# Performance work log

Hardware: AMD Instinct MI355X
Metric: run time of the kernel (lower is better)

The kernel has to match this reference:

```python
import jax, jax.numpy as jnp
import numpy as np

BATCH, NODE, IN_DIM, DIM, TOPK = 256, 256, 64, 64, 20
EPS = 1e-5
NEG_SLOPE = 0.2


def setup_inputs() -> dict:
    key = jax.random.key(0)
    ks = jax.random.split(key, 10)
    z, o = jnp.zeros, jnp.ones
    return {
        "data": jax.random.normal(ks[0], (BATCH, NODE, IN_DIM), jnp.float32),
        "emb_table": jax.random.normal(ks[1], (NODE, DIM), jnp.float32) * 0.1,
        "lin_w": jax.random.normal(ks[2], (IN_DIM, DIM), jnp.float32) * 0.05,
        "att_i": jax.random.normal(ks[3], (DIM,), jnp.float32) * 0.1,
        "att_j": jax.random.normal(ks[4], (DIM,), jnp.float32) * 0.1,
        "att_em_i": jax.random.normal(ks[5], (DIM,), jnp.float32) * 0.1,
        "att_em_j": jax.random.normal(ks[6], (DIM,), jnp.float32) * 0.1,
        "gnn_bias": z((DIM,), jnp.float32),
        "bn1_gamma": o((DIM,), jnp.float32), "bn1_beta": z((DIM,), jnp.float32),
        "bn2_gamma": o((DIM,), jnp.float32), "bn2_beta": z((DIM,), jnp.float32),
        "enc_w": jax.random.normal(ks[7], (NODE * DIM, DIM), jnp.float32) * 0.01,
        "enc_b": z((DIM,), jnp.float32),
        "arr_w": jax.random.normal(ks[8], (DIM, 7), jnp.float32) * 0.1,
        "arr_b": z((7,), jnp.float32),
        "out_w": jax.random.normal(ks[9], (DIM, 1), jnp.float32) * 0.1,
        "out_b": z((1,), jnp.float32),
    }


def _batchnorm(x, gamma, beta, axes):
    # BatchNorm1d in training mode: batch statistics
    mean = jnp.mean(x, axis=axes, keepdims=True)
    var = jnp.var(x, axis=axes, keepdims=True)
    return (x - mean) * jax.lax.rsqrt(var + EPS) * gamma + beta


def _gdn_forward(data, emb_table, lin_w, att_i, att_j, att_em_i, att_em_j, gnn_bias,
                 bn1_gamma, bn1_beta, bn2_gamma, bn2_beta,
                 enc_w, enc_b, arr_w, arr_b, out_w, out_b):
    B, N, F = data.shape
    BN = B * N
    x = data.reshape(BN, F)

    # learned graph: top-k cosine similarity of (detached) node embeddings
    w = jax.lax.stop_gradient(emb_table)
    nrm = jnp.linalg.norm(w, axis=-1)
    cos = (w @ w.T) / (nrm[:, None] * nrm[None, :])
    topk_idx = jax.lax.top_k(cos, TOPK)[1]                 # [N, TOPK]

    # gated_edge_index = (gated_j=sources, gated_i=targets), batched with +b*N offset
    src1 = topk_idx.reshape(-1)                            # sources (j)
    dst1 = jnp.repeat(jnp.arange(N), TOPK)                 # targets (i)
    offs = (jnp.arange(B) * N)[:, None]
    src = (src1[None, :] + offs).reshape(-1)               # [B*N*TOPK]
    dst = (dst1[None, :] + offs).reshape(-1)

    # PyG: remove_self_loops then add_self_loops -> mask duplicate self edges,
    # append exactly one self loop per node
    loop = jnp.arange(BN)
    src_all = jnp.concatenate([src, loop])
    dst_all = jnp.concatenate([dst, loop])
    valid = jnp.concatenate([src != dst, jnp.ones((BN,), bool)])

    # GraphLayer (GAT-style, heads=1, concat=False)
    xl = x @ lin_w                                         # [BN, DIM]
    emb_rep = jnp.tile(emb_table, (B, 1))                  # [BN, DIM] (embedding.repeat(B,1))
    x_i, x_j = xl[dst_all], xl[src_all]                    # per-edge gathers
    e_i, e_j = emb_rep[dst_all], emb_rep[src_all]
    logits = (x_i @ att_i) + (e_i @ att_em_i) + (x_j @ att_j) + (e_j @ att_em_j)
    logits = jnp.where(logits >= 0, logits, NEG_SLOPE * logits)  # leaky_relu(0.2)
    logits = jnp.where(valid, logits, -1e9)

    # segment softmax over incoming edges of each target node
    seg_max = jax.ops.segment_max(logits, dst_all, num_segments=BN)
    a = jnp.where(valid, jnp.exp(logits - seg_max[dst_all]), 0.0)
    denom = jax.ops.segment_sum(a, dst_all, num_segments=BN)
    alpha = a / denom[dst_all]

    # weighted scatter-add aggregation + bias, then GNNLayer BN + ReLU
    agg = jax.ops.segment_sum(x_j * alpha[:, None], dst_all, num_segments=BN) + gnn_bias
    gnn_out = jax.nn.relu(_batchnorm(agg, bn1_gamma, bn1_beta, axes=(0,)))

    x3 = gnn_out.reshape(B, N, -1)                         # [B, N, DIM]
    encoded = x3.reshape(B, -1) @ enc_w + enc_b            # [B, DIM]
    arrangement = encoded @ arr_w + arr_b                  # [B, 7]

    y = x3 * emb_table[None]                               # mul by node embeddings
    y = jnp.transpose(y, (0, 2, 1))                        # [B, DIM, N]
    y = jax.nn.relu(_batchnorm(y, bn2_gamma[None, :, None], bn2_beta[None, :, None], axes=(0, 2)))
    y = jnp.transpose(y, (0, 2, 1))                        # [B, N, DIM] (dropout is identity in eval)
    score = (y @ out_w + out_b).reshape(B, N)              # OutLayer (layer_num=1) + view(-1, N)
    return score, arrangement


def reference(data, emb_table, lin_w, att_i, att_j, att_em_i, att_em_j, gnn_bias,
              bn1_gamma, bn1_beta, bn2_gamma, bn2_beta,
              enc_w, enc_b, arr_w, arr_b, out_w, out_b):
    return _gdn_forward(data, emb_table, lin_w, att_i, att_j, att_em_i, att_em_j, gnn_bias,
                        bn1_gamma, bn1_beta, bn2_gamma, bn2_beta,
                        enc_w, enc_b, arr_w, arr_b, out_w, out_b)
```

## Files before the change

### kernel.cpp

```cpp
#include <hip/hip_runtime.h>
#include <hip/hip_bf16.h>

#define TK 20
#define BN 65536

typedef const float* fpc;
typedef __attribute__((ext_vector_type(8))) short short8;
typedef __attribute__((ext_vector_type(4))) float floatx4;

__device__ __forceinline__ short f2b(float f){
  unsigned u = __float_as_uint(f);
  return (short)((u + 0x7fffu + ((u >> 16) & 1u)) >> 16);
}
__device__ __forceinline__ float b2fu(unsigned short u){
  return __uint_as_float(((unsigned)u) << 16);
}

__global__ void __launch_bounds__(256) k_gx(fpc data, fpc emb, fpc lin_w, fpc att_i, fpc att_j,
        fpc att_em_i, fpc att_em_j,
        int* __restrict__ topk, float* __restrict__ emi, float* __restrict__ emj,
        __hip_bfloat16* __restrict__ xl, float* __restrict__ aip, float* __restrict__ ajp,
        float* __restrict__ bnsum){
  __shared__ float s_cos[256];
  __shared__ float s_wi[64];
  const int t = threadIdx.x, w = t >> 6, lane = t & 63;

  if (blockIdx.x < 256){
    if (blockIdx.x == 0){
      #pragma unroll
      for (int i = 0; i < 8; ++i) bnsum[t + i*256] = 0.f;
    }
    const int i = blockIdx.x;
    if (t < 64) s_wi[t] = emb[i*64 + t];
    __syncthreads();
    float dot = 0.f, nj = 0.f, ni = 0.f;
    for (int f = 0; f < 64; ++f){
      float wj = emb[t*64 + f], wi = s_wi[f];
      dot = fmaf(wi, wj, dot); nj = fmaf(wj, wj, nj); ni = fmaf(wi, wi, ni);
    }
    s_cos[t] = dot / (sqrtf(ni) * sqrtf(nj));
    __syncthreads();
    if (t < 64){
      float v0 = s_cos[t], v1 = s_cos[t+64], v2 = s_cos[t+128], v3 = s_cos[t+192];
      int taken = 0;
      for (int r = 0; r < TK; ++r){
        float bv = (taken & 1) ? -3.f : v0; int bi = t;
        float c;
        c = (taken & 2) ? -3.f : v1; if (c > bv){ bv = c; bi = t+64;  }
        c = (taken & 4) ? -3.f : v2; if (c > bv){ bv = c; bi = t+128; }
        c = (taken & 8) ? -3.f : v3; if (c > bv){ bv = c; bi = t+192; }
        for (int m = 1; m < 64; m <<= 1){
          float ov = __shfl_xor(bv, m, 64);
          int   oi = __shfl_xor(bi, m, 64);
          if (ov > bv || (ov == bv && oi < bi)){ bv = ov; bi = oi; }
        }
        if (t == 0) topk[i*TK + r] = bi;
        if ((bi & 63) == t) taken |= 1 << (bi >> 6);
      }
    } else if (t < 128){
      int d = t - 64;
      float wv = s_wi[d];
      float p1 = wv * att_em_i[d];
      float p2 = wv * att_em_j[d];
      for (int m = 1; m < 64; m <<= 1){
        p1 += __shfl_xor(p1, m, 64);
        p2 += __shfl_xor(p2, m, 64);
      }
      if (d == 0){ emi[i] = p1; emj[i] = p2; }
    }
    return;
  }

  const int m = lane & 15, quad = lane >> 4;
  short8 B[4][2];
  #pragma unroll
  for (int ct = 0; ct < 4; ++ct)
    #pragma unroll
    for (int kc = 0; kc < 2; ++kc)
      #pragma unroll
      for (int j = 0; j < 8; ++j)
        B[ct][kc][j] = f2b(lin_w[(kc*32 + quad*8 + j)*64 + ct*16 + m]);

  const int rw = (blockIdx.x - 256)*64 + w*16;
  short8 A0, A1;
  {
    const float4* ap0 = (const float4*)(data + (size_t)(rw + m)*64 + quad*8);
    float4 q0 = ap0[0], q1 = ap0[1];
    A0[0]=f2b(q0.x); A0[1]=f2b(q0.y); A0[2]=f2b(q0.z); A0[3]=f2b(q0.w);
    A0[4]=f2b(q1.x); A0[5]=f2b(q1.y); A0[6]=f2b(q1.z); A0[7]=f2b(q1.w);
    const float4* ap1 = (const float4*)(data + (size_t)(rw + m)*64 + 32 + quad*8);
    float4 q2 = ap1[0], q3 = ap1[1];
    A1[0]=f2b(q2.x); A1[1]=f2b(q2.y); A1[2]=f2b(q2.z); A1[3]=f2b(q2.w);
    A1[4]=f2b(q3.x); A1[5]=f2b(q3.y); A1[6]=f2b(q3.z); A1[7]=f2b(q3.w);
  }
  floatx4 acc[4];
  #pragma unroll
  for (int ct = 0; ct < 4; ++ct){
    floatx4 z = {0.f, 0.f, 0.f, 0.f};
    acc[ct] = __builtin_amdgcn_mfma_f32_16x16x32_bf16(A0, B[ct][0], z, 0, 0, 0);
    acc[ct] = __builtin_amdgcn_mfma_f32_16x16x32_bf16(A1, B[ct][1], acc[ct], 0, 0, 0);
  }
  float p1[4] = {0.f,0.f,0.f,0.f}, p2[4] = {0.f,0.f,0.f,0.f};
  #pragma unroll
  for (int ct = 0; ct < 4; ++ct){
    const float wi = att_i[ct*16 + m], wj = att_j[ct*16 + m];
    #pragma unroll
    for (int reg = 0; reg < 4; ++reg){
      float v = acc[ct][reg];
      const int row = rw + quad*4 + reg;
      xl[(size_t)row*64 + ct*16 + m] = __float2bfloat16(v);
      p1[reg] = fmaf(v, wi, p1[reg]);
      p2[reg] = fmaf(v, wj, p2[reg]);
    }
  }
  #pragma unroll
  for (int reg = 0; reg < 4; ++reg){
    #pragma unroll
    for (int s = 1; s < 16; s <<= 1){
      p1[reg] += __shfl_xor(p1[reg], s, 16);
      p2[reg] += __shfl_xor(p2[reg], s, 16);
    }
    if (m == 0){
      const int r = rw + quad*4 + reg;
      aip[r] = p1[reg];
      ajp[r] = p2[reg];
    }
  }
}

__global__ void __launch_bounds__(256) k_attn_agg(const int* __restrict__ topk,
                         const __hip_bfloat16* __restrict__ xl,
                         fpc aip, fpc ajp, fpc emi_g, fpc emj_g, fpc gnn_bias,
                         __hip_bfloat16* __restrict__ agg, float* __restrict__ bnsum){
  __shared__ float s_alpha[4][32];
  __shared__ int   s_src[4][32];
  __shared__ float s_ps[4][64], s_pq[4][64];
  const int t = threadIdx.x, w = t >> 6, lane = t & 63;
  const float bias = gnn_bias[lane];
  const int vbase = blockIdx.x*64 + w*16;
  float sum = 0.f, sq = 0.f;
  for (int j = 0; j < 16; ++j){
    const int v = vbase + j, i = v & 255, b = v >> 8;
    float lg = -1e30f; int sl = 0;
    if (lane < 21){
      sl = (lane < 20) ? topk[i*TK + lane] : i;
      if (lane == 20 || sl != i){
        float l = aip[v] + emi_g[i] + ajp[b*256 + sl] + emj_g[sl];
        lg = (l >= 0.f) ? l : 0.2f*l;
      }
    }
    float m = lg;
    for (int s = 1; s < 32; s <<= 1) m = fmaxf(m, __shfl_xor(m, s, 32));
    float e = (lg > -1e29f) ? __expf(lg - m) : 0.f;
    float den = e;
    for (int s = 1; s < 32; s <<= 1) den += __shfl_xor(den, s, 32);
    if (lane < 21){ s_alpha[w][lane] = e / den; s_src[w][lane] = b*256 + sl; }
    float acc = bias;
    #pragma unroll
    for (int k = 0; k < 21; ++k)
      acc = fmaf(s_alpha[w][k], __bfloat162float(xl[(size_t)s_src[w][k]*64 + lane]), acc);
    agg[(size_t)v*64 + lane] = __float2bfloat16(acc);
    sum += acc; sq = fmaf(acc, acc, sq);
  }
  s_ps[w][lane] = sum; s_pq[w][lane] = sq;
  __syncthreads();
  if (t < 64){
    const int cp = (blockIdx.x & 7)*64;
    atomicAdd(&bnsum[cp + t],       s_ps[0][t] + s_ps[1][t] + s_ps[2][t] + s_ps[3][t]);
    atomicAdd(&bnsum[512 + cp + t], s_pq[0][t] + s_pq[1][t] + s_pq[2][t] + s_pq[3][t]);
  }
}

__global__ void __launch_bounds__(256) k_encst(const __hip_bfloat16* __restrict__ agg, fpc enc_w,
                         fpc emb, fpc g1, fpc be1,
                         float* __restrict__ bnsum, float* __restrict__ part){
  const int t = threadIdx.x;

  if (blockIdx.x < 256){
    const int w = t >> 6, lane = t & 63;
    const int m = lane & 15, quad = lane >> 4;
    const int kt = blockIdx.x & 127, bt = blockIdx.x >> 7, kbase = kt*128;
    float scA[8], shA[8], scB[8], shB[8];
    #pragma unroll
    for (int j = 0; j < 8; ++j){
      #pragma unroll
      for (int par = 0; par < 2; ++par){
        const int d = par*32 + quad*8 + j;
        float S = 0.f, Q = 0.f;
        #pragma unroll
        for (int cp = 0; cp < 8; ++cp){ S += bnsum[cp*64 + d]; Q += bnsum[512 + cp*64 + d]; }
        float mean = S * (1.f/BN);
        float var  = Q * (1.f/BN) - mean*mean;
        float sc = g1[d] * rsqrtf(var + 1e-5f);
        float sh = be1[d] - mean*sc;
        if (par == 0){ scA[j] = sc; shA[j] = sh; } else { scB[j] = sc; shB[j] = sh; }
      }
    }
    floatx4 acc[2][4];
    #pragma unroll
    for (int i = 0; i < 2; ++i)
      #pragma unroll
      for (int ct = 0; ct < 4; ++ct)
        acc[i][ct] = (floatx4){0.f, 0.f, 0.f, 0.f};

    #pragma unroll
    for (int kc = 0; kc < 4; ++kc){
      const int kof = kbase + kc*32 + quad*8;
      const bool odd = (kc & 1);
      short8 Bf[4];
      #pragma unroll
      for (int ct = 0; ct < 4; ++ct)
        #pragma unroll
        for (int j = 0; j < 8; ++j)
          Bf[ct][j] = f2b(enc_w[(size_t)(kof + j)*64 + ct*16 + m]);
      #pragma unroll
      for (int i = 0; i < 2; ++i){
        const int row = bt*128 + (w*2 + i)*16 + m;
        uint4 uu = *(const uint4*)((const unsigned short*)agg + (size_t)row*16384 + kof);
        unsigned short h[8] = {
          (unsigned short)(uu.x & 0xffff), (unsigned short)(uu.x >> 16),
          (unsigned short)(uu.y & 0xffff), (unsigned short)(uu.y >> 16),
          (unsigned short)(uu.z & 0xffff), (unsigned short)(uu.z >> 16),
          (unsigned short)(uu.w & 0xffff), (unsigned short)(uu.w >> 16) };
        short8 Af;
        if (!odd){
          #pragma unroll
          for (int j = 0; j < 8; ++j) Af[j] = f2b(fmaxf(fmaf(b2fu(h[j]), scA[j], shA[j]), 0.f));
        } else {
          #pragma unroll
          for (int j = 0; j < 8; ++j) Af[j] = f2b(fmaxf(fmaf(b2fu(h[j]), scB[j], shB[j]), 0.f));
        }
        #pragma unroll
        for (int ct = 0; ct < 4; ++ct)
          acc[i][ct] = __builtin_amdgcn_mfma_f32_16x16x32_bf16(Af, Bf[ct], acc[i][ct], 0, 0, 0);
      }
    }
    #pragma unroll
    for (int i = 0; i < 2; ++i)
      #pragma unroll
      for (int ct = 0; ct < 4; ++ct)
        #pragma unroll
        for (int reg = 0; reg < 4; ++reg){
          const int row = bt*128 + (w*2 + i)*16 + quad*4 + reg;
          part[(size_t)kt*16384 + row*64 + ct*16 + m] = acc[i][ct][reg];
        }
    return;
  }

  const int sb = blockIdx.x - 256;
  const int qc = t & 15, rs = t >> 4;
  float4 sc, sh;
  {
    float s[4], q[4];
    #pragma unroll
    for (int k = 0; k < 4; ++k){
      const int d = qc*4 + k;
      float S = 0.f, Q = 0.f;
      #pragma unroll
      for (int cp = 0; cp < 8; ++cp){ S += bnsum[cp*64 + d]; Q += bnsum[512 + cp*64 + d]; }
      float mean = S * (1.f/BN);
      float var  = Q * (1.f/BN) - mean*mean;
      s[k] = g1[d] * rsqrtf(var + 1e-5f);
      q[k] = be1[d] - mean*s[k];
    }
    sc = make_float4(s[0], s[1], s[2], s[3]);
    sh = make_float4(q[0], q[1], q[2], q[3]);
  }
  const float4* emb4 = (const float4*)emb;
  float4 ys = make_float4(0,0,0,0), yq = make_float4(0,0,0,0);
  const int rbase = sb*32;
  #pragma unroll
  for (int jj = 0; jj < 2; ++jj){
    const int r = rbase + jj*16 + rs;
    ushort4 u = *(const ushort4*)((const unsigned short*)agg + (size_t)r*64 + qc*4);
    float4 e = emb4[(r & 255)*16 + qc];
    float4 y;
    y.x = fmaxf(fmaf(b2fu(u.x), sc.x, sh.x), 0.f) * e.x;
    y.y = fmaxf(fmaf(b2fu(u.y), sc.y, sh.y), 0.f) * e.y;
    y.z = fmaxf(fmaf(b2fu(u.z), sc.z, sh.z), 0.f) * e.z;
    y.w = fmaxf(fmaf(b2fu(u.w), sc.w, sh.w), 0.f) * e.w;
    ys.x += y.x; ys.y += y.y; ys.z += y.z; ys.w += y.w;
    yq.x = fmaf(y.x, y.x, yq.x); yq.y = fmaf(y.y, y.y, yq.y);
    yq.z = fmaf(y.z, y.z, yq.z); yq.w = fmaf(y.w, y.w, yq.w);
  }
  __shared__ float4 s_s[16][16], s_q[16][16];
  s_s[rs][qc] = ys; s_q[rs][qc] = yq;
  __syncthreads();
  if (t < 64){
    const int qq = t >> 2, comp = t & 3;
    float S = 0.f, Q = 0.f;
    #pragma unroll
    for (int rr = 0; rr < 16; ++rr){
      S += ((const float*)&s_s[rr][qq])[comp];
      Q += ((const float*)&s_q[rr][qq])[comp];
    }
    const int cp = (sb & 7)*64;
    atomicAdd(&bnsum[1024 + cp + t], S);
    atomicAdd(&bnsum[1536 + cp + t], Q);
  }
}

__global__ void __launch_bounds__(256) k_fin(const float* __restrict__ part,
                      const __hip_bfloat16* __restrict__ agg, fpc emb,
                      fpc g1, fpc be1, fpc g2, fpc be2,
                      const float* __restrict__ bnsum,
                      fpc enc_b, fpc arr_w, fpc arr_b, fpc out_w, fpc out_b,
                      float* __restrict__ out){
  const int t = threadIdx.x;

  if (blockIdx.x < 256){
    __shared__ float s_enc[4][64];
    const int b = blockIdx.x, w = t >> 6, lane = t & 63;
    float s = 0.f;
    #pragma unroll 8
    for (int k = 0; k < 32; ++k)
      s += part[(size_t)(w*32 + k)*16384 + b*64 + lane];
    s_enc[w][lane] = s;
    __syncthreads();
    if (t < 64){
      float e = s_enc[0][t] + s_enc[1][t] + s_enc[2][t] + s_enc[3][t] + enc_b[t];
      float o[7];
      #pragma unroll
      for (int j = 0; j < 7; ++j) o[j] = e * arr_w[t*7 + j];
      #pragma unroll
      for (int j = 0; j < 7; ++j)
        #pragma unroll
        for (int m = 1; m < 64; m <<= 1) o[j] += __shfl_xor(o[j], m, 64);
      if (t == 0){
        #pragma unroll
        for (int j = 0; j < 7; ++j) out[65536 + b*7 + j] = o[j] + arr_b[j];
      }
    }
    return;
  }

  const int w = t >> 6, lane = t & 63;
  const int qc = lane & 15, rq = lane >> 4;
  float sc1[4], sh1[4], sc2[4], sh2[4], ow[4];
  #pragma unroll
  for (int k = 0; k < 4; ++k){
    const int d = qc*4 + k;
    float S1 = 0.f, Q1 = 0.f, S2 = 0.f, Q2 = 0.f;
    #pragma unroll
    for (int cp = 0; cp < 8; ++cp){
      S1 += bnsum[cp*64 + d];        Q1 += bnsum[512 + cp*64 + d];
      S2 += bnsum[1024 + cp*64 + d]; Q2 += bnsum[1536 + cp*64 + d];
    }
    float m1 = S1 * (1.f/BN), v1 = Q1 * (1.f/BN) - m1*m1;
    sc1[k] = g1[d] * rsqrtf(v1 + 1e-5f);
    sh1[k] = be1[d] - m1*sc1[k];
    float m2 = S2 * (1.f/BN), v2 = Q2 * (1.f/BN) - m2*m2;
    sc2[k] = g2[d] * rsqrtf(v2 + 1e-5f);
    sh2[k] = be2[d] - m2*sc2[k];
    ow[k]  = out_w[d];
  }
  const float ob = out_b[0];
  const float4* emb4 = (const float4*)emb;
  const int base = (blockIdx.x - 256)*32 + w*8;
  #pragma unroll
  for (int it = 0; it < 2; ++it){
    const int r = base + it*4 + rq;
    ushort4 u = *(const ushort4*)((const unsigned short*)agg + (size_t)r*64 + qc*4);
    float4 e4 = emb4[(r & 255)*16 + qc];
    float p = 0.f, g, y, yh;
    g = fmaxf(fmaf(b2fu(u.x), sc1[0], sh1[0]), 0.f); y = g*e4.x;
    yh = fmaxf(fmaf(y, sc2[0], sh2[0]), 0.f); p = fmaf(yh, ow[0], p);
    g = fmaxf(fmaf(b2fu(u.y), sc1[1], sh1[1]), 0.f); y = g*e4.y;
    yh = fmaxf(fmaf(y, sc2[1], sh2[1]), 0.f); p = fmaf(yh, ow[1], p);
    g = fmaxf(fmaf(b2fu(u.z), sc1[2], sh1[2]), 0.f); y = g*e4.z;
    yh = fmaxf(fmaf(y, sc2[2], sh2[2]), 0.f); p = fmaf(yh, ow[2], p);
    g = fmaxf(fmaf(b2fu(u.w), sc1[3], sh1[3]), 0.f); y = g*e4.w;
    yh = fmaxf(fmaf(y, sc2[3], sh2[3]), 0.f); p = fmaf(yh, ow[3], p);
    #pragma unroll
    for (int mm = 1; mm < 16; mm <<= 1) p += __shfl_xor(p, mm, 16);
    if (qc == 0) out[r] = p + ob;
  }
}

extern "C" void kernel_launch(void* const* d_in, const int* in_sizes, int n_in,
                              void* d_out, int out_size, void* d_ws, size_t ws_size,
                              hipStream_t stream) {
  fpc data     = (fpc)d_in[0];
  fpc emb      = (fpc)d_in[1];
  fpc lin_w    = (fpc)d_in[2];
  fpc att_i    = (fpc)d_in[3];
  fpc att_j    = (fpc)d_in[4];
  fpc att_em_i = (fpc)d_in[5];
  fpc att_em_j = (fpc)d_in[6];
  fpc gnn_bias = (fpc)d_in[7];
  fpc g1       = (fpc)d_in[8];
  fpc be1      = (fpc)d_in[9];
  fpc g2       = (fpc)d_in[10];
  fpc be2      = (fpc)d_in[11];
  fpc enc_w    = (fpc)d_in[12];
  fpc enc_b    = (fpc)d_in[13];
  fpc arr_w    = (fpc)d_in[14];
  fpc arr_b    = (fpc)d_in[15];
  fpc out_w    = (fpc)d_in[16];
  fpc out_b    = (fpc)d_in[17];

  float* fw = (float*)d_ws;
  int*   topk    = (int*)d_ws;
  float* emi     = fw + 5120;
  float* emj     = fw + 5376;
  float* bnsum   = fw + 5632;
  float* aip     = fw + 7680;
  float* ajp     = fw + 73216;
  __hip_bfloat16* agg = (__hip_bfloat16*)(fw + 138752);
  __hip_bfloat16* xl  = (__hip_bfloat16*)(fw + 2235904);
  float* part    = (float*)xl;
  float* out     = (float*)d_out;

  k_gx       <<<1280,  256, 0, stream>>>(data, emb, lin_w, att_i, att_j, att_em_i, att_em_j,
                                         topk, emi, emj, xl, aip, ajp, bnsum);
  k_attn_agg <<<1024,  256, 0, stream>>>(topk, xl, aip, ajp, emi, emj, gnn_bias, agg, bnsum);
  k_encst    <<<2304,  256, 0, stream>>>(agg, enc_w, emb, g1, be1, bnsum, part);
  k_fin      <<<2304,  256, 0, stream>>>(part, agg, emb, g1, be1, g2, be2, bnsum,
                                         enc_b, arr_w, arr_b, out_w, out_b, out);
}
```

Baseline: 174.9 us.

## Stage per-batch xl slice, topk and attention terms in LDS for aggregation

Each block now cooperatively loads the full 256x64 bf16 feature slice of its batch, its 64 nodes' topk indices, and precombined attention logit terms into shared memory. The gather loop then reads neighbours from LDS instead of issuing scattered global loads. This targets the latency of irregular global gathers. In exchange, each block uses roughly 39 KB of LDS, which lowers occupancy, and every block re-reads the whole batch slice, so each slice is loaded four times.

```diff
diff --git a/kernel.cpp b/kernel.cpp
--- a/kernel.cpp
+++ b/kernel.cpp
@@ -132,20 +132,41 @@
                          const __hip_bfloat16* __restrict__ xl,
                          fpc aip, fpc ajp, fpc emi_g, fpc emj_g, fpc gnn_bias,
                          __hip_bfloat16* __restrict__ agg, float* __restrict__ bnsum){
+  __shared__ __hip_bfloat16 s_xl[256*64];
+  __shared__ int   s_topk[64*TK];
+  __shared__ float s_aj[256];
+  __shared__ float s_ai[64];
   __shared__ float s_alpha[4][32];
   __shared__ int   s_src[4][32];
   __shared__ float s_ps[4][64], s_pq[4][64];
   const int t = threadIdx.x, w = t >> 6, lane = t & 63;
+  const int b  = blockIdx.x >> 2;
+  const int i0 = (blockIdx.x & 3) * 64;
   const float bias = gnn_bias[lane];
+
+  {
+    const uint4* src4 = (const uint4*)(xl + (size_t)b*16384);
+    uint4* dst4 = (uint4*)s_xl;
+    #pragma unroll
+    for (int k = 0; k < 8; ++k) dst4[t + k*256] = src4[t + k*256];
+    #pragma unroll
+    for (int k = 0; k < 5; ++k) s_topk[t + k*256] = topk[(size_t)i0*TK + t + k*256];
+    s_aj[t] = ajp[b*256 + t] + emj_g[t];
+    if (t < 64) s_ai[t] = aip[(size_t)blockIdx.x*64 + t] + emi_g[i0 + t];
+  }
+  __syncthreads();
+
   const int vbase = blockIdx.x*64 + w*16;
   float sum = 0.f, sq = 0.f;
   for (int j = 0; j < 16; ++j){
-    const int v = vbase + j, i = v & 255, b = v >> 8;
+    const int nloc = w*16 + j;
+    const int i = i0 + nloc;
+    const float an = s_ai[nloc];
     float lg = -1e30f; int sl = 0;
     if (lane < 21){
-      sl = (lane < 20) ? topk[i*TK + lane] : i;
+      sl = (lane < 20) ? s_topk[nloc*TK + lane] : i;
       if (lane == 20 || sl != i){
-        float l = aip[v] + emi_g[i] + ajp[b*256 + sl] + emj_g[sl];
+        float l = an + s_aj[sl];
         lg = (l >= 0.f) ? l : 0.2f*l;
       }
     }
@@ -154,12 +175,12 @@
     float e = (lg > -1e29f) ? __expf(lg - m) : 0.f;
     float den = e;
     for (int s = 1; s < 32; s <<= 1) den += __shfl_xor(den, s, 32);
-    if (lane < 21){ s_alpha[w][lane] = e / den; s_src[w][lane] = b*256 + sl; }
+    if (lane < 21){ s_alpha[w][lane] = e / den; s_src[w][lane] = sl; }
     float acc = bias;
     #pragma unroll
     for (int k = 0; k < 21; ++k)
-      acc = fmaf(s_alpha[w][k], __bfloat162float(xl[(size_t)s_src[w][k]*64 + lane]), acc);
-    agg[(size_t)v*64 + lane] = __float2bfloat16(acc);
+      acc = fmaf(s_alpha[w][k], __bfloat162float(s_xl[s_src[w][k]*64 + lane]), acc);
+    agg[(size_t)(vbase + j)*64 + lane] = __float2bfloat16(acc);
     sum += acc; sq = fmaf(acc, acc, sq);
   }
   s_ps[w][lane] = sum; s_pq[w][lane] = sq;
```

Result: slower. 178.9 us (+2.3%).
